# Kernel tuning notes

Hardware: AMD Instinct MI355X
Metric: run time of the kernel (lower is better)

## Reference

```python
import jax, jax.numpy as jnp
import numpy as np

NEG_SLOPE = 0.2

def setup_inputs() -> dict:
    key = jax.random.key(0)
    k1, k2, k3, k4 = jax.random.split(key, 4)
    N, K, C_IN, C_OUT = 8192, 4, 512, 512
    inputs = jax.random.normal(k1, (N, C_IN), dtype=jnp.float32)
    adj_set = jax.random.uniform(k2, (K, N, N), dtype=jnp.float32)
    att = jax.random.uniform(k3, (K,), dtype=jnp.float32)
    # xavier_uniform for w
    limit = float(np.sqrt(6.0 / (C_IN + C_OUT)))
    w = jax.random.uniform(k4, (C_IN, C_OUT), minval=-limit, maxval=limit, dtype=jnp.float32)
    b = jnp.zeros((C_OUT,), dtype=jnp.float32)
    return {"inputs": inputs, "adj_set": adj_set, "att": att, "w": w, "b": b}

def reference(inputs, adj_set, att, w, b):
    # support: [N, C_out]
    support = inputs @ w + b
    # residual=True path: outputs = sum_i att[i] * (adj_i @ support)
    #                             = (sum_i att[i] * adj_i) @ support
    combined_adj = jnp.einsum('k,knm->nm', att, adj_set)  # [N, N]
    outputs = combined_adj @ support                       # [N, C_out]
    # LeakyReLU(negative_slope=0.2)
    return jnp.where(outputs >= 0, outputs, NEG_SLOPE * outputs)
```

## Files before the change

kernel.cpp:

```cpp
#include <hip/hip_runtime.h>

#define LP  40
#define LPB 40

typedef __attribute__((ext_vector_type(8))) short short8;
typedef __attribute__((ext_vector_type(4))) short short4t;
typedef __attribute__((ext_vector_type(4))) float f32x4;

__device__ __forceinline__ short f2bf(float f) {
  unsigned u = __builtin_bit_cast(unsigned, f);
  u += 0x7FFFu + ((u >> 16) & 1u);
  return (short)(u >> 16);
}

__device__ __forceinline__ float lrelu(float v) { return v >= 0.f ? v : 0.2f * v; }

__global__ __launch_bounds__(256) void k_wt(const float* __restrict__ w,
                                            short* __restrict__ wt) {
  __shared__ float t[64][65];
  int c0 = (blockIdx.x & 7) * 64;
  int n0 = (blockIdx.x >> 3) * 64;
  int r  = threadIdx.x >> 4;
  int q4 = (threadIdx.x & 15) * 4;
  for (int i = 0; i < 4; i++) {
    int c = r + i * 16;
    f32x4 v = *(const f32x4*)(w + (size_t)(c0 + c) * 512 + (n0 + q4));
    t[c][q4 + 0] = v[0]; t[c][q4 + 1] = v[1]; t[c][q4 + 2] = v[2]; t[c][q4 + 3] = v[3];
  }
  __syncthreads();
  for (int i = 0; i < 4; i++) {
    int n = r + i * 16;
    short4t o;
    for (int j = 0; j < 4; j++) o[j] = f2bf(t[q4 + j][n]);
    *(short4t*)(wt + (size_t)(n0 + n) * 512 + (c0 + q4)) = o;
  }
}

__global__ __launch_bounds__(512, 2) void k_support(const float* __restrict__ inp,
                                                    const short* __restrict__ wt,
                                                    const float* __restrict__ bias,
                                                    short* __restrict__ sup) {
  __shared__ __align__(16) short As[512 * LP];
  __shared__ __align__(16) short Bs[64 * LP];
  const int tid = threadIdx.x;
  const int m0 = blockIdx.x * 64;
  const int wave = tid >> 6, lane = tid & 63;
  const int wn = wave >> 1, wm = wave & 1;
  const int lr = lane & 15, lk = lane >> 4;
  const int bm = tid >> 3, bk = (tid & 7) * 4;
  f32x4 acc[8][2] = {};
  short8 ar[4]; f32x4 br;
  auto loadA = [&](int s) {
    const short* p = wt + (size_t)tid * 512 + s * 32;
    ar[0] = *(const short8*)(p);      ar[1] = *(const short8*)(p + 8);
    ar[2] = *(const short8*)(p + 16); ar[3] = *(const short8*)(p + 24);
  };
  auto loadB = [&](int s) {
    br = *(const f32x4*)(inp + (size_t)(m0 + bm) * 512 + s * 32 + bk);
  };
  loadA(0); loadB(0);
  for (int s = 0; s < 16; s++) {
    short* ad = As + tid * LP;
    *(short8*)(ad) = ar[0]; *(short8*)(ad + 8) = ar[1];
    *(short8*)(ad + 16) = ar[2]; *(short8*)(ad + 24) = ar[3];
    short4t bo;
    for (int j = 0; j < 4; j++) bo[j] = f2bf(br[j]);
    *(short4t*)(Bs + bm * LP + bk) = bo;
    __syncthreads();
    if (s + 1 < 16) { loadA(s + 1); loadB(s + 1); }
    short8 af[8], bfr[2];
    for (int nf = 0; nf < 8; nf++)
      af[nf] = *(const short8*)(As + (wn * 128 + nf * 16 + lr) * LP + lk * 8);
    for (int mf = 0; mf < 2; mf++)
      bfr[mf] = *(const short8*)(Bs + (wm * 32 + mf * 16 + lr) * LP + lk * 8);
    for (int nf = 0; nf < 8; nf++)
      for (int mf = 0; mf < 2; mf++)
        acc[nf][mf] = __builtin_amdgcn_mfma_f32_16x16x32_bf16(af[nf], bfr[mf], acc[nf][mf], 0, 0, 0);
    __syncthreads();
  }
  for (int nf = 0; nf < 8; nf++) {
    int nb = wn * 128 + nf * 16 + lk * 4;
    for (int mf = 0; mf < 2; mf++) {
      int m = m0 + wm * 32 + mf * 16 + lr;
      for (int j = 0; j < 4; j++) {
        int n = nb + j;
        sup[(size_t)n * 8192 + m] = f2bf(acc[nf][mf][j] + bias[n]);
      }
    }
  }
}

#define ISSUE(SL, S) {                                                          \
    const float* p_ = abase + (size_t)(S) * 32;                                 \
    R[SL][0] = __builtin_nontemporal_load((const f32x4*)(p_));                  \
    R[SL][1] = __builtin_nontemporal_load((const f32x4*)(p_ + (1ull << 26)));   \
    R[SL][2] = __builtin_nontemporal_load((const f32x4*)(p_ + (2ull << 26)));   \
    R[SL][3] = __builtin_nontemporal_load((const f32x4*)(p_ + (3ull << 26)));   \
  }

#define ISSUEAF(SL, S) {                                                        \
    const short* q_ = supp + (size_t)(S) * 32;                                  \
    AF[SL][0] = *(const short8*)(q_);                                           \
    AF[SL][1] = *(const short8*)(q_ + (size_t)16 * 8192);                       \
    AF[SL][2] = *(const short8*)(q_ + (size_t)32 * 8192);                       \
    AF[SL][3] = *(const short8*)(q_ + (size_t)48 * 8192);                       \
  }

#define STEP(U) {                                                               \
    ISSUE(((U) + 2) & 3, (s0 + (U) + 2) & (nsteps - 1))                         \
    ISSUEAF(((U) + 1) & 1, (s0 + (U) + 1) & (nsteps - 1))                       \
    __builtin_amdgcn_sched_barrier(0);                                          \
    asm volatile("s_waitcnt vmcnt(20)" ::: "memory");                           \
    __builtin_amdgcn_sched_barrier(0);                                          \
    f32x4 c_;                                                                   \
    _Pragma("unroll") for (int e = 0; e < 4; e++)                               \
      c_[e] = t0 * R[(U) & 3][0][e] + t1 * R[(U) & 3][1][e]                     \
            + t2 * R[(U) & 3][2][e] + t3 * R[(U) & 3][3][e];                    \
    short4t o_;                                                                 \
    _Pragma("unroll") for (int e = 0; e < 4; e++) o_[e] = f2bf(c_[e]);          \
    *(short4t*)(Bs[(U) & 1] + r * LPB + q * 4) = o_;                            \
    asm volatile("s_waitcnt lgkmcnt(0)" ::: "memory");                          \
    __builtin_amdgcn_sched_barrier(0);                                          \
    __builtin_amdgcn_s_barrier();                                               \
    __builtin_amdgcn_sched_barrier(0);                                          \
    short8 bfr[4];                                                              \
    _Pragma("unroll") for (int mf = 0; mf < 4; mf++)                            \
      bfr[mf] = *(const short8*)(Bs[(U) & 1] + (mf * 16 + lr) * LPB + lk * 8);  \
    asm volatile("s_waitcnt vmcnt(8)" ::: "memory");                            \
    __builtin_amdgcn_sched_barrier(0);                                          \
    _Pragma("unroll") for (int nf = 0; nf < 4; nf++)                            \
      _Pragma("unroll") for (int mf = 0; mf < 4; mf++)                          \
        acc[nf][mf] = __builtin_amdgcn_mfma_f32_16x16x32_bf16(AF[(U) & 1][nf],  \
                          bfr[mf], acc[nf][mf], 0, 0, 0);                       \
  }

__global__ __launch_bounds__(512, 2) void k_main(const float* __restrict__ adj,
                                                 const float* __restrict__ att,
                                                 const short* __restrict__ sup,
                                                 float* __restrict__ part,
                                                 float* __restrict__ outp,
                                                 int ksplit) {
  __shared__ __align__(16) short Bs[2][64 * LPB];
  const int tid = threadIdx.x;
  const int b = blockIdx.x;
  const int xpk = 8 / ksplit;
  const int xcd = b & 7;
  const int kc = xcd / xpk;
  const int m0 = ((b >> 3) * xpk + (xcd % xpk)) * 64;
  const int kchunk = 8192 / ksplit;
  const int nsteps = kchunk / 32;
  const int kbase = kc * kchunk;
  const float t0 = att[0], t1 = att[1], t2 = att[2], t3 = att[3];
  const int wave = tid >> 6, lane = tid & 63;
  const int lr = lane & 15, lk = lane >> 4;
  const int r = tid >> 3, q = tid & 7;
  f32x4 acc[4][4] = {};
  const float* abase = adj + (size_t)(m0 + r) * 8192 + kbase + q * 4;
  const short* supp = sup + (size_t)(wave * 64 + lr) * 8192 + kbase + lk * 8;
  f32x4 R[4][4];
  short8 AF[2][4];

  ISSUE(0, 0) ISSUEAF(0, 0) ISSUE(1, 1)
  for (int s0 = 0; s0 < nsteps; s0 += 4) {
    STEP(0) STEP(1) STEP(2) STEP(3)
  }

#pragma unroll
  for (int nf = 0; nf < 4; nf++) {
    int n = wave * 64 + nf * 16 + lk * 4;
#pragma unroll
    for (int mf = 0; mf < 4; mf++) {
      int m = m0 + mf * 16 + lr;
      f32x4 v = acc[nf][mf];
      if (ksplit == 1) {
        for (int j = 0; j < 4; j++) v[j] = lrelu(v[j]);
        __builtin_nontemporal_store(v, (f32x4*)(outp + (size_t)m * 512 + n));
      } else {
        __builtin_nontemporal_store(v, (f32x4*)(part + ((size_t)kc << 22) + (size_t)m * 512 + n));
      }
    }
  }
}

__global__ __launch_bounds__(256) void k_reduce(const float* __restrict__ part,
                                                float* __restrict__ outp, int ksplit) {
  const size_t total = (size_t)8192 * 512 / 4;
  for (size_t i = (size_t)blockIdx.x * 256 + threadIdx.x; i < total;
       i += (size_t)gridDim.x * 256) {
    f32x4 a = __builtin_nontemporal_load((const f32x4*)(part + i * 4));
    for (int k = 1; k < ksplit; k++) {
      f32x4 bv = __builtin_nontemporal_load((const f32x4*)(part + ((size_t)k << 22) + i * 4));
      for (int j = 0; j < 4; j++) a[j] += bv[j];
    }
    f32x4 v;
    for (int j = 0; j < 4; j++) v[j] = lrelu(a[j]);
    __builtin_nontemporal_store(v, (f32x4*)(outp + i * 4));
  }
}

extern "C" void kernel_launch(void* const* d_in, const int* in_sizes, int n_in,
                              void* d_out, int out_size, void* d_ws, size_t ws_size,
                              hipStream_t stream) {
  const float* inputs = (const float*)d_in[0];
  const float* adj    = (const float*)d_in[1];
  const float* att    = (const float*)d_in[2];
  const float* w      = (const float*)d_in[3];
  const float* bias   = (const float*)d_in[4];
  float* outp = (float*)d_out;

  char* ws = (char*)d_ws;
  short* sup  = (short*)(ws);
  short* wt   = (short*)(ws + (8u << 20));
  float* part = (float*)(ws + (9u << 20));

  const size_t base = (9ull << 20), psz = (1ull << 24);
  int ksplit = (ws_size >= base + 2 * psz) ? 2 : 1;

  k_wt<<<64, 256, 0, stream>>>(w, wt);
  k_support<<<128, 512, 0, stream>>>(inputs, wt, bias, sup);
  k_main<<<128 * ksplit, 512, 0, stream>>>(adj, att, sup, part, outp, ksplit);
  if (ksplit > 1) k_reduce<<<1024, 256, 0, stream>>>(part, outp, ksplit);
}
```

Measured before the change: 308.1 us.

## Add 128-row tile main kernel with 4-way K split and reduction

Adds a new main kernel in which each block handles 128 output rows (instead of 64) over a quarter of the K dimension. The kernel uses a shallower two-stage register prefetch and wider 8-float adjacency loads per thread. Doubling the row tile halves how often the support matrix is re-read per adjacency byte, and the 4-way K split keeps 256 blocks in flight. The cost is more accumulator registers, a larger partial buffer, and a four-way reduction pass. The old path remains as a fallback when the workspace is too small.

```diff
diff --git a/kernel.cpp b/kernel.cpp
--- a/kernel.cpp
+++ b/kernel.cpp
@@ -90,7 +90,89 @@
   }
 }
 
-#define ISSUE(SL, S) {                                                          \
+#define ISSUEB(SL, S) {                                                         \
+    const float* p_ = abase + (size_t)(S) * 32;                                 \
+    R[SL][0][0] = __builtin_nontemporal_load((const f32x4*)(p_));               \
+    R[SL][0][1] = __builtin_nontemporal_load((const f32x4*)(p_ + 4));           \
+    R[SL][1][0] = __builtin_nontemporal_load((const f32x4*)(p_ + (1ull << 26)));\
+    R[SL][1][1] = __builtin_nontemporal_load((const f32x4*)(p_ + (1ull << 26) + 4));\
+    R[SL][2][0] = __builtin_nontemporal_load((const f32x4*)(p_ + (2ull << 26)));\
+    R[SL][2][1] = __builtin_nontemporal_load((const f32x4*)(p_ + (2ull << 26) + 4));\
+    R[SL][3][0] = __builtin_nontemporal_load((const f32x4*)(p_ + (3ull << 26)));\
+    R[SL][3][1] = __builtin_nontemporal_load((const f32x4*)(p_ + (3ull << 26) + 4));\
+  }
+
+#define STEPB(U) {                                                              \
+    const int s_ = s0 + (U);                                                    \
+    _Pragma("unroll") for (int nf = 0; nf < 4; nf++)                            \
+      AF[nf] = *(const short8*)(supp + (size_t)(nf * 16) * 8192 + (size_t)s_ * 32); \
+    ISSUEB(((U) + 1) & 1, (s_ + 1) & 63)                                        \
+    __builtin_amdgcn_sched_barrier(0);                                          \
+    asm volatile("s_waitcnt vmcnt(8)" ::: "memory");                            \
+    __builtin_amdgcn_sched_barrier(0);                                          \
+    f32x4 c0_, c1_;                                                             \
+    _Pragma("unroll") for (int e = 0; e < 4; e++) {                             \
+      c0_[e] = t0 * R[(U)][0][0][e] + t1 * R[(U)][1][0][e]                      \
+             + t2 * R[(U)][2][0][e] + t3 * R[(U)][3][0][e];                     \
+      c1_[e] = t0 * R[(U)][0][1][e] + t1 * R[(U)][1][1][e]                      \
+             + t2 * R[(U)][2][1][e] + t3 * R[(U)][3][1][e];                     \
+    }                                                                           \
+    short8 o_;                                                                  \
+    _Pragma("unroll") for (int e = 0; e < 4; e++) {                             \
+      o_[e] = f2bf(c0_[e]); o_[4 + e] = f2bf(c1_[e]);                           \
+    }                                                                           \
+    *(short8*)(Bs[(U) & 1] + r * LPB + q * 8) = o_;                             \
+    asm volatile("s_waitcnt lgkmcnt(0)" ::: "memory");                          \
+    __builtin_amdgcn_sched_barrier(0);                                          \
+    __builtin_amdgcn_s_barrier();                                               \
+    __builtin_amdgcn_sched_barrier(0);                                          \
+    _Pragma("unroll") for (int mf = 0; mf < 8; mf++) {                          \
+      short8 bfr = *(const short8*)(Bs[(U) & 1] + (mf * 16 + lr) * LPB + lk * 8); \
+      _Pragma("unroll") for (int nf = 0; nf < 4; nf++)                          \
+        acc[nf][mf] = __builtin_amdgcn_mfma_f32_16x16x32_bf16(AF[nf], bfr,      \
+                                                              acc[nf][mf], 0, 0, 0); \
+    }                                                                           \
+  }
+
+__global__ __launch_bounds__(512, 2) void k_main128(const float* __restrict__ adj,
+                                                    const float* __restrict__ att,
+                                                    const short* __restrict__ sup,
+                                                    float* __restrict__ part) {
+  __shared__ __align__(16) short Bs[2][128 * LPB];
+  const int tid = threadIdx.x;
+  const int b = blockIdx.x;
+  const int xcd = b & 7;
+  const int kc = xcd >> 1;
+  const int m0 = ((b >> 3) * 2 + (xcd & 1)) * 128;
+  const int kbase = kc * 2048;
+  const float t0 = att[0], t1 = att[1], t2 = att[2], t3 = att[3];
+  const int wave = tid >> 6, lane = tid & 63;
+  const int lr = lane & 15, lk = lane >> 4;
+  const int r = tid >> 2, q = tid & 3;
+  f32x4 acc[4][8] = {};
+  const float* abase = adj + (size_t)(m0 + r) * 8192 + kbase + q * 8;
+  const short* supp = sup + (size_t)(wave * 64 + lr) * 8192 + kbase + lk * 8;
+  f32x4 R[2][4][2];
+  short8 AF[4];
+
+  ISSUEB(0, 0)
+  for (int s0 = 0; s0 < 64; s0 += 2) {
+    STEPB(0) STEPB(1)
+  }
+
+#pragma unroll
+  for (int nf = 0; nf < 4; nf++) {
+    int n = wave * 64 + nf * 16 + lk * 4;
+#pragma unroll
+    for (int mf = 0; mf < 8; mf++) {
+      int m = m0 + mf * 16 + lr;
+      __builtin_nontemporal_store(acc[nf][mf],
+          (f32x4*)(part + ((size_t)kc << 22) + (size_t)m * 512 + n));
+    }
+  }
+}
+
+#define ISSUE64(SL, S) {                                                        \
     const float* p_ = abase + (size_t)(S) * 32;                                 \
     R[SL][0] = __builtin_nontemporal_load((const f32x4*)(p_));                  \
     R[SL][1] = __builtin_nontemporal_load((const f32x4*)(p_ + (1ull << 26)));   \
@@ -98,7 +180,7 @@
     R[SL][3] = __builtin_nontemporal_load((const f32x4*)(p_ + (3ull << 26)));   \
   }
 
-#define ISSUEAF(SL, S) {                                                        \
+#define ISSUEAF64(SL, S) {                                                      \
     const short* q_ = supp + (size_t)(S) * 32;                                  \
     AF[SL][0] = *(const short8*)(q_);                                           \
     AF[SL][1] = *(const short8*)(q_ + (size_t)16 * 8192);                       \
@@ -106,9 +188,9 @@
     AF[SL][3] = *(const short8*)(q_ + (size_t)48 * 8192);                       \
   }
 
-#define STEP(U) {                                                               \
-    ISSUE(((U) + 2) & 3, (s0 + (U) + 2) & (nsteps - 1))                         \
-    ISSUEAF(((U) + 1) & 1, (s0 + (U) + 1) & (nsteps - 1))                       \
+#define STEP64(U) {                                                             \
+    ISSUE64(((U) + 2) & 3, (s0 + (U) + 2) & (nsteps - 1))                       \
+    ISSUEAF64(((U) + 1) & 1, (s0 + (U) + 1) & (nsteps - 1))                     \
     __builtin_amdgcn_sched_barrier(0);                                          \
     asm volatile("s_waitcnt vmcnt(20)" ::: "memory");                           \
     __builtin_amdgcn_sched_barrier(0);                                          \
@@ -134,12 +216,12 @@
                           bfr[mf], acc[nf][mf], 0, 0, 0);                       \
   }
 
-__global__ __launch_bounds__(512, 2) void k_main(const float* __restrict__ adj,
-                                                 const float* __restrict__ att,
-                                                 const short* __restrict__ sup,
-                                                 float* __restrict__ part,
-                                                 float* __restrict__ outp,
-                                                 int ksplit) {
+__global__ __launch_bounds__(512, 2) void k_main64(const float* __restrict__ adj,
+                                                   const float* __restrict__ att,
+                                                   const short* __restrict__ sup,
+                                                   float* __restrict__ part,
+                                                   float* __restrict__ outp,
+                                                   int ksplit) {
   __shared__ __align__(16) short Bs[2][64 * LPB];
   const int tid = threadIdx.x;
   const int b = blockIdx.x;
@@ -160,9 +242,9 @@
   f32x4 R[4][4];
   short8 AF[2][4];
 
-  ISSUE(0, 0) ISSUEAF(0, 0) ISSUE(1, 1)
+  ISSUE64(0, 0) ISSUEAF64(0, 0) ISSUE64(1, 1)
   for (int s0 = 0; s0 < nsteps; s0 += 4) {
-    STEP(0) STEP(1) STEP(2) STEP(3)
+    STEP64(0) STEP64(1) STEP64(2) STEP64(3)
   }
 
 #pragma unroll
@@ -214,10 +296,16 @@
   float* part = (float*)(ws + (9u << 20));
 
   const size_t base = (9ull << 20), psz = (1ull << 24);
-  int ksplit = (ws_size >= base + 2 * psz) ? 2 : 1;
 
   k_wt<<<64, 256, 0, stream>>>(w, wt);
   k_support<<<128, 512, 0, stream>>>(inputs, wt, bias, sup);
-  k_main<<<128 * ksplit, 512, 0, stream>>>(adj, att, sup, part, outp, ksplit);
-  if (ksplit > 1) k_reduce<<<1024, 256, 0, stream>>>(part, outp, ksplit);
-}
+
+  if (ws_size >= base + 4 * psz) {
+    k_main128<<<256, 512, 0, stream>>>(adj, att, sup, part);
+    k_reduce<<<1024, 256, 0, stream>>>(part, outp, 4);
+  } else {
+    int ksplit = (ws_size >= base + 2 * psz) ? 2 : 1;
+    k_main64<<<128 * ksplit, 512, 0, stream>>>(adj, att, sup, part, outp, ksplit);
+    if (ksplit > 1) k_reduce<<<1024, 256, 0, stream>>>(part, outp, ksplit);
+  }
+}
```

After: 342.9 us. +11.3%, slower.

## Double K-step to 64 per iteration with wider loads and templated split

Applied to the files above, without the earlier changes.

The main GEMM loop now handles 64 columns of K per step instead of 32. Each thread loads 8 floats per adjacency slice, writes one 16-byte bf16 store into LDS, and runs twice as many MFMAs between barriers. The number of in-flight register buffers changes from 4 slots to 2, and the split factor becomes a template parameter so the step count is a compile-time constant. The intent is to halve barrier and wait overhead per unit of work and to use wider memory transactions. In exchange, register pressure rises and pipelining depth in steps drops.

```diff
diff --git a/kernel.cpp b/kernel.cpp
--- a/kernel.cpp
+++ b/kernel.cpp
@@ -1,7 +1,7 @@
 #include <hip/hip_runtime.h>
 
 #define LP  40
-#define LPB 40
+#define LPB 72
 
 typedef __attribute__((ext_vector_type(8))) short short8;
 typedef __attribute__((ext_vector_type(4))) short short4t;
@@ -90,79 +90,92 @@
   }
 }
 
-#define ISSUE(SL, S) {                                                          \
-    const float* p_ = abase + (size_t)(S) * 32;                                 \
+#define ISSUEA(SL, S) {                                                         \
+    const float* p_ = abase + (size_t)(S) * 64;                                 \
     R[SL][0] = __builtin_nontemporal_load((const f32x4*)(p_));                  \
-    R[SL][1] = __builtin_nontemporal_load((const f32x4*)(p_ + (1ull << 26)));   \
-    R[SL][2] = __builtin_nontemporal_load((const f32x4*)(p_ + (2ull << 26)));   \
-    R[SL][3] = __builtin_nontemporal_load((const f32x4*)(p_ + (3ull << 26)));   \
-  }
-
-#define ISSUEAF(SL, S) {                                                        \
-    const short* q_ = supp + (size_t)(S) * 32;                                  \
-    AF[SL][0] = *(const short8*)(q_);                                           \
-    AF[SL][1] = *(const short8*)(q_ + (size_t)16 * 8192);                       \
-    AF[SL][2] = *(const short8*)(q_ + (size_t)32 * 8192);                       \
-    AF[SL][3] = *(const short8*)(q_ + (size_t)48 * 8192);                       \
-  }
-
-#define STEP(U) {                                                               \
-    ISSUE(((U) + 2) & 3, (s0 + (U) + 2) & (nsteps - 1))                         \
-    ISSUEAF(((U) + 1) & 1, (s0 + (U) + 1) & (nsteps - 1))                       \
-    __builtin_amdgcn_sched_barrier(0);                                          \
-    asm volatile("s_waitcnt vmcnt(20)" ::: "memory");                           \
-    __builtin_amdgcn_sched_barrier(0);                                          \
-    f32x4 c_;                                                                   \
-    _Pragma("unroll") for (int e = 0; e < 4; e++)                               \
-      c_[e] = t0 * R[(U) & 3][0][e] + t1 * R[(U) & 3][1][e]                     \
-            + t2 * R[(U) & 3][2][e] + t3 * R[(U) & 3][3][e];                    \
-    short4t o_;                                                                 \
-    _Pragma("unroll") for (int e = 0; e < 4; e++) o_[e] = f2bf(c_[e]);          \
-    *(short4t*)(Bs[(U) & 1] + r * LPB + q * 4) = o_;                            \
+    R[SL][1] = __builtin_nontemporal_load((const f32x4*)(p_ + 4));              \
+    R[SL][2] = __builtin_nontemporal_load((const f32x4*)(p_ + (1ull << 26)));   \
+    R[SL][3] = __builtin_nontemporal_load((const f32x4*)(p_ + (1ull << 26) + 4));\
+    R[SL][4] = __builtin_nontemporal_load((const f32x4*)(p_ + (2ull << 26)));   \
+    R[SL][5] = __builtin_nontemporal_load((const f32x4*)(p_ + (2ull << 26) + 4));\
+    R[SL][6] = __builtin_nontemporal_load((const f32x4*)(p_ + (3ull << 26)));   \
+    R[SL][7] = __builtin_nontemporal_load((const f32x4*)(p_ + (3ull << 26) + 4));\
+  }
+
+#define ISSUEF(SL, S) {                                                         \
+    const short* q_ = supp + (size_t)(S) * 64;                                  \
+    AF[SL][0][0] = *(const short8*)(q_);                                        \
+    AF[SL][0][1] = *(const short8*)(q_ + 32);                                   \
+    AF[SL][1][0] = *(const short8*)(q_ + (size_t)16 * 8192);                    \
+    AF[SL][1][1] = *(const short8*)(q_ + (size_t)16 * 8192 + 32);               \
+    AF[SL][2][0] = *(const short8*)(q_ + (size_t)32 * 8192);                    \
+    AF[SL][2][1] = *(const short8*)(q_ + (size_t)32 * 8192 + 32);               \
+    AF[SL][3][0] = *(const short8*)(q_ + (size_t)48 * 8192);                    \
+    AF[SL][3][1] = *(const short8*)(q_ + (size_t)48 * 8192 + 32);               \
+  }
+
+#define STEPK(U) {                                                              \
+    const int s_ = s0 + (U);                                                    \
+    ISSUEF(((U) + 1) & 1, (s_ + 1) & (NSTEPS - 1))                              \
+    __builtin_amdgcn_sched_barrier(0);                                          \
+    asm volatile("s_waitcnt vmcnt(16)" ::: "memory");                           \
+    __builtin_amdgcn_sched_barrier(0);                                          \
+    f32x4 cA_, cB_;                                                             \
+    _Pragma("unroll") for (int e = 0; e < 4; e++) {                             \
+      cA_[e] = t0 * R[(U)][0][e] + t1 * R[(U)][2][e]                            \
+             + t2 * R[(U)][4][e] + t3 * R[(U)][6][e];                           \
+      cB_[e] = t0 * R[(U)][1][e] + t1 * R[(U)][3][e]                            \
+             + t2 * R[(U)][5][e] + t3 * R[(U)][7][e];                           \
+    }                                                                           \
+    short8 o_;                                                                  \
+    _Pragma("unroll") for (int e = 0; e < 4; e++) {                             \
+      o_[e] = f2bf(cA_[e]); o_[4 + e] = f2bf(cB_[e]);                           \
+    }                                                                           \
+    *(short8*)(Bs[(U)] + r * LPB + q * 8) = o_;                                 \
+    ISSUEA((U), (s_ + 2) & (NSTEPS - 1))                                        \
+    __builtin_amdgcn_sched_barrier(0);                                          \
     asm volatile("s_waitcnt lgkmcnt(0)" ::: "memory");                          \
     __builtin_amdgcn_sched_barrier(0);                                          \
     __builtin_amdgcn_s_barrier();                                               \
     __builtin_amdgcn_sched_barrier(0);                                          \
-    short8 bfr[4];                                                              \
-    _Pragma("unroll") for (int mf = 0; mf < 4; mf++)                            \
-      bfr[mf] = *(const short8*)(Bs[(U) & 1] + (mf * 16 + lr) * LPB + lk * 8);  \
-    asm volatile("s_waitcnt vmcnt(8)" ::: "memory");                            \
-    __builtin_amdgcn_sched_barrier(0);                                          \
-    _Pragma("unroll") for (int nf = 0; nf < 4; nf++)                            \
-      _Pragma("unroll") for (int mf = 0; mf < 4; mf++)                          \
-        acc[nf][mf] = __builtin_amdgcn_mfma_f32_16x16x32_bf16(AF[(U) & 1][nf],  \
-                          bfr[mf], acc[nf][mf], 0, 0, 0);                       \
-  }
-
+    _Pragma("unroll") for (int h = 0; h < 2; h++) {                             \
+      _Pragma("unroll") for (int mf = 0; mf < 4; mf++) {                        \
+        short8 bfr = *(const short8*)(Bs[(U)] + (mf * 16 + lr) * LPB + h * 32 + lk * 8); \
+        _Pragma("unroll") for (int nf = 0; nf < 4; nf++)                        \
+          acc[nf][mf] = __builtin_amdgcn_mfma_f32_16x16x32_bf16(                \
+              AF[(U)][nf][h], bfr, acc[nf][mf], 0, 0, 0);                       \
+      }                                                                         \
+    }                                                                           \
+  }
+
+template <int KSPLIT>
 __global__ __launch_bounds__(512, 2) void k_main(const float* __restrict__ adj,
                                                  const float* __restrict__ att,
                                                  const short* __restrict__ sup,
                                                  float* __restrict__ part,
-                                                 float* __restrict__ outp,
-                                                 int ksplit) {
+                                                 float* __restrict__ outp) {
+  constexpr int NSTEPS = 8192 / KSPLIT / 64;
   __shared__ __align__(16) short Bs[2][64 * LPB];
   const int tid = threadIdx.x;
   const int b = blockIdx.x;
-  const int xpk = 8 / ksplit;
+  const int xpk = 8 / KSPLIT;
   const int xcd = b & 7;
   const int kc = xcd / xpk;
   const int m0 = ((b >> 3) * xpk + (xcd % xpk)) * 64;
-  const int kchunk = 8192 / ksplit;
-  const int nsteps = kchunk / 32;
-  const int kbase = kc * kchunk;
+  const int kbase = kc * (8192 / KSPLIT);
   const float t0 = att[0], t1 = att[1], t2 = att[2], t3 = att[3];
   const int wave = tid >> 6, lane = tid & 63;
   const int lr = lane & 15, lk = lane >> 4;
   const int r = tid >> 3, q = tid & 7;
   f32x4 acc[4][4] = {};
-  const float* abase = adj + (size_t)(m0 + r) * 8192 + kbase + q * 4;
+  const float* abase = adj + (size_t)(m0 + r) * 8192 + kbase + q * 8;
   const short* supp = sup + (size_t)(wave * 64 + lr) * 8192 + kbase + lk * 8;
-  f32x4 R[4][4];
-  short8 AF[2][4];
-
-  ISSUE(0, 0) ISSUEAF(0, 0) ISSUE(1, 1)
-  for (int s0 = 0; s0 < nsteps; s0 += 4) {
-    STEP(0) STEP(1) STEP(2) STEP(3)
+  f32x4 R[2][8];
+  short8 AF[2][4][2];
+
+  ISSUEA(0, 0) ISSUEF(0, 0) ISSUEA(1, 1)
+  for (int s0 = 0; s0 < NSTEPS; s0 += 2) {
+    STEPK(0) STEPK(1)
   }
 
 #pragma unroll
@@ -172,7 +185,7 @@
     for (int mf = 0; mf < 4; mf++) {
       int m = m0 + mf * 16 + lr;
       f32x4 v = acc[nf][mf];
-      if (ksplit == 1) {
+      if (KSPLIT == 1) {
         for (int j = 0; j < 4; j++) v[j] = lrelu(v[j]);
         __builtin_nontemporal_store(v, (f32x4*)(outp + (size_t)m * 512 + n));
       } else {
@@ -214,10 +227,14 @@
   float* part = (float*)(ws + (9u << 20));
 
   const size_t base = (9ull << 20), psz = (1ull << 24);
-  int ksplit = (ws_size >= base + 2 * psz) ? 2 : 1;
 
   k_wt<<<64, 256, 0, stream>>>(w, wt);
   k_support<<<128, 512, 0, stream>>>(inputs, wt, bias, sup);
-  k_main<<<128 * ksplit, 512, 0, stream>>>(adj, att, sup, part, outp, ksplit);
-  if (ksplit > 1) k_reduce<<<1024, 256, 0, stream>>>(part, outp, ksplit);
-}
+
+  if (ws_size >= base + 2 * psz) {
+    k_main<2><<<256, 512, 0, stream>>>(adj, att, sup, part, outp);
+    k_reduce<<<1024, 256, 0, stream>>>(part, outp, 2);
+  } else {
+    k_main<1><<<128, 512, 0, stream>>>(adj, att, sup, part, outp);
+  }
+}
```

After: 336.9 us. 1.09x slower.

## Add producer/consumer warp-specialized main kernel using global-to-LDS loads

Applied to the files above, without the earlier changes.

Adds a new main kernel in which wave 0 streams the four adjacency slices straight into a 4-slot LDS ring with global_load_lds, while the other waves wait on shared flags, combine the slices with the attention weights, convert to bf16 and run MFMAs. Counters in LDS tell the producer when a slot is free. The aim is to hide HBM latency for the 1 GiB adjacency stream without staging it through registers, and to spread the combine work across all waves. The risks are spin-wait overhead, a single producer wave possibly limiting load issue rate, and 128 KB of LDS per block, which may cut occupancy below the two blocks the launch bounds request.

```diff
diff --git a/kernel.cpp b/kernel.cpp
--- a/kernel.cpp
+++ b/kernel.cpp
@@ -90,25 +90,144 @@
   }
 }
 
-#define ISSUE(SL, S) {                                                          \
+__global__ __launch_bounds__(512, 2) void k_pc(const float* __restrict__ adj,
+                                               const float* __restrict__ att,
+                                               const short* __restrict__ sup,
+                                               float* __restrict__ part) {
+  constexpr int NSTEPS = 128;
+  __shared__ __align__(16) float ring[4][8192];
+  __shared__ int flg[4];
+  __shared__ int done[4];
+  const int tid = threadIdx.x;
+  const int b = blockIdx.x;
+  const int xcd = b & 7;
+  const int kc = xcd >> 2;
+  const int m0 = ((b >> 3) * 4 + (xcd & 3)) * 64;
+  const int kbase = kc * 4096;
+  const float t0 = att[0], t1 = att[1], t2 = att[2], t3 = att[3];
+  const int wv = tid >> 6, lane = tid & 63;
+  const int lr = lane & 15, lk = lane >> 4;
+  const int swz = (lane & 7) << 4;
+  volatile int* vflg = flg;
+  volatile int* vdone = done;
+
+  if (tid < 4) { flg[tid] = 0; done[tid] = 0; }
+  __syncthreads();
+
+  const short* sb = sup + (size_t)(wv * 64 + lr) * 8192 + kbase + lk * 8;
+  f32x4 acc[4][4] = {};
+  short8 af[4], afn[4];
+
+  const int lr8 = lane >> 3, l7 = lane & 7;
+  const float* pbase = adj + (size_t)(m0 + lr8) * 8192 + kbase + (l7 ^ lr8) * 4;
+
+#define PISSUE(S, SLOT)                                                        \
+  _Pragma("unroll") for (int c = 0; c < 32; c++) {                             \
+    const float* g_ = pbase + (((size_t)(c >> 3)) << 26)                       \
+                    + (size_t)((c & 7) * 8) * 8192 + (size_t)(S) * 32;         \
+    __builtin_amdgcn_global_load_lds(                                          \
+        (const __attribute__((address_space(1))) unsigned*)g_,                 \
+        (__attribute__((address_space(3))) unsigned*)((char*)ring[SLOT] + c * 1024), \
+        16, 0, 0);                                                             \
+  }
+
+#define LOADAF(DST, S)                                                         \
+  _Pragma("unroll") for (int nf = 0; nf < 4; nf++)                             \
+    DST[nf] = *(const short8*)(sb + (size_t)(nf * 16) * 8192 + (size_t)(S) * 32);
+
+#define CONSUME(S, AFC)                                                        \
+  {                                                                            \
+    const char* rb_ = (const char*)ring[(S) & 3];                              \
+    _Pragma("unroll") for (int mf = 0; mf < 4; mf++) {                         \
+      const char* rr_ = rb_ + (mf * 16 + lr) * 128;                            \
+      const int o0_ = (lk * 32) ^ swz, o1_ = (lk * 32 + 16) ^ swz;             \
+      f32x4 r0a = *(const f32x4*)(rr_ + o0_);                                  \
+      f32x4 r0b = *(const f32x4*)(rr_ + o1_);                                  \
+      f32x4 r1a = *(const f32x4*)(rr_ + 8192 + o0_);                           \
+      f32x4 r1b = *(const f32x4*)(rr_ + 8192 + o1_);                           \
+      f32x4 r2a = *(const f32x4*)(rr_ + 16384 + o0_);                          \
+      f32x4 r2b = *(const f32x4*)(rr_ + 16384 + o1_);                          \
+      f32x4 r3a = *(const f32x4*)(rr_ + 24576 + o0_);                          \
+      f32x4 r3b = *(const f32x4*)(rr_ + 24576 + o1_);                          \
+      short8 bfr_;                                                             \
+      _Pragma("unroll") for (int e = 0; e < 4; e++) {                          \
+        bfr_[e]     = f2bf(t0 * r0a[e] + t1 * r1a[e] + t2 * r2a[e] + t3 * r3a[e]); \
+        bfr_[4 + e] = f2bf(t0 * r0b[e] + t1 * r1b[e] + t2 * r2b[e] + t3 * r3b[e]); \
+      }                                                                        \
+      _Pragma("unroll") for (int nf = 0; nf < 4; nf++)                         \
+        acc[nf][mf] = __builtin_amdgcn_mfma_f32_16x16x32_bf16(AFC[nf], bfr_,   \
+                                                              acc[nf][mf], 0, 0, 0); \
+    }                                                                          \
+  }
+
+  if (wv == 0) {
+    PISSUE(0, 0)
+    LOADAF(af, 0)
+    for (int s = 0; s < NSTEPS; s++) {
+      const int sn = s + 1;
+      if (sn < NSTEPS) {
+        const int slot = sn & 3;
+        const int need = 7 * (sn >> 2);
+        while (vdone[slot] < need) __builtin_amdgcn_s_sleep(2);
+        asm volatile("" ::: "memory");
+        PISSUE(sn, slot)
+        LOADAF(afn, sn)
+        asm volatile("s_waitcnt vmcnt(36)" ::: "memory");
+      } else {
+        asm volatile("s_waitcnt vmcnt(0)" ::: "memory");
+      }
+      vflg[s & 3] = s + 1;
+      asm volatile("" ::: "memory");
+      CONSUME(s, af)
+#pragma unroll
+      for (int nf = 0; nf < 4; nf++) af[nf] = afn[nf];
+    }
+  } else {
+    LOADAF(af, 0)
+    for (int s = 0; s < NSTEPS; s++) {
+      if (s + 1 < NSTEPS) LOADAF(afn, s + 1)
+      while (vflg[s & 3] != s + 1) __builtin_amdgcn_s_sleep(2);
+      asm volatile("" ::: "memory");
+      CONSUME(s, af)
+      asm volatile("" ::: "memory");
+      if (lane == 0) atomicAdd(&done[s & 3], 1);
+#pragma unroll
+      for (int nf = 0; nf < 4; nf++) af[nf] = afn[nf];
+    }
+  }
+
+#pragma unroll
+  for (int nf = 0; nf < 4; nf++) {
+    int n = wv * 64 + nf * 16 + lk * 4;
+#pragma unroll
+    for (int mf = 0; mf < 4; mf++) {
+      int m = m0 + mf * 16 + lr;
+      __builtin_nontemporal_store(acc[nf][mf],
+          (f32x4*)(part + ((size_t)kc << 22) + (size_t)m * 512 + n));
+    }
+  }
+#undef PISSUE
+#undef LOADAF
+#undef CONSUME
+}
+
+#define ISSUE64(SL, S) {                                                        \
     const float* p_ = abase + (size_t)(S) * 32;                                 \
     R[SL][0] = __builtin_nontemporal_load((const f32x4*)(p_));                  \
     R[SL][1] = __builtin_nontemporal_load((const f32x4*)(p_ + (1ull << 26)));   \
     R[SL][2] = __builtin_nontemporal_load((const f32x4*)(p_ + (2ull << 26)));   \
     R[SL][3] = __builtin_nontemporal_load((const f32x4*)(p_ + (3ull << 26)));   \
   }
-
-#define ISSUEAF(SL, S) {                                                        \
+#define ISSUEAF64(SL, S) {                                                      \
     const short* q_ = supp + (size_t)(S) * 32;                                  \
     AF[SL][0] = *(const short8*)(q_);                                           \
     AF[SL][1] = *(const short8*)(q_ + (size_t)16 * 8192);                       \
     AF[SL][2] = *(const short8*)(q_ + (size_t)32 * 8192);                       \
     AF[SL][3] = *(const short8*)(q_ + (size_t)48 * 8192);                       \
   }
-
-#define STEP(U) {                                                               \
-    ISSUE(((U) + 2) & 3, (s0 + (U) + 2) & (nsteps - 1))                         \
-    ISSUEAF(((U) + 1) & 1, (s0 + (U) + 1) & (nsteps - 1))                       \
+#define STEP64(U) {                                                             \
+    ISSUE64(((U) + 2) & 3, (s0 + (U) + 2) & (nsteps - 1))                       \
+    ISSUEAF64(((U) + 1) & 1, (s0 + (U) + 1) & (nsteps - 1))                     \
     __builtin_amdgcn_sched_barrier(0);                                          \
     asm volatile("s_waitcnt vmcnt(20)" ::: "memory");                           \
     __builtin_amdgcn_sched_barrier(0);                                          \
@@ -134,12 +253,12 @@
                           bfr[mf], acc[nf][mf], 0, 0, 0);                       \
   }
 
-__global__ __launch_bounds__(512, 2) void k_main(const float* __restrict__ adj,
-                                                 const float* __restrict__ att,
-                                                 const short* __restrict__ sup,
-                                                 float* __restrict__ part,
-                                                 float* __restrict__ outp,
-                                                 int ksplit) {
+__global__ __launch_bounds__(512, 2) void k_main64(const float* __restrict__ adj,
+                                                   const float* __restrict__ att,
+                                                   const short* __restrict__ sup,
+                                                   float* __restrict__ part,
+                                                   float* __restrict__ outp,
+                                                   int ksplit) {
   __shared__ __align__(16) short Bs[2][64 * LPB];
   const int tid = threadIdx.x;
   const int b = blockIdx.x;
@@ -159,12 +278,10 @@
   const short* supp = sup + (size_t)(wave * 64 + lr) * 8192 + kbase + lk * 8;
   f32x4 R[4][4];
   short8 AF[2][4];
-
-  ISSUE(0, 0) ISSUEAF(0, 0) ISSUE(1, 1)
+  ISSUE64(0, 0) ISSUEAF64(0, 0) ISSUE64(1, 1)
   for (int s0 = 0; s0 < nsteps; s0 += 4) {
-    STEP(0) STEP(1) STEP(2) STEP(3)
-  }
-
+    STEP64(0) STEP64(1) STEP64(2) STEP64(3)
+  }
 #pragma unroll
   for (int nf = 0; nf < 4; nf++) {
     int n = wave * 64 + nf * 16 + lk * 4;
@@ -214,10 +331,14 @@
   float* part = (float*)(ws + (9u << 20));
 
   const size_t base = (9ull << 20), psz = (1ull << 24);
-  int ksplit = (ws_size >= base + 2 * psz) ? 2 : 1;
 
   k_wt<<<64, 256, 0, stream>>>(w, wt);
   k_support<<<128, 512, 0, stream>>>(inputs, wt, bias, sup);
-  k_main<<<128 * ksplit, 512, 0, stream>>>(adj, att, sup, part, outp, ksplit);
-  if (ksplit > 1) k_reduce<<<1024, 256, 0, stream>>>(part, outp, ksplit);
-}
+
+  if (ws_size >= base + 2 * psz) {
+    k_pc<<<256, 512, 0, stream>>>(adj, att, sup, part);
+    k_reduce<<<1024, 256, 0, stream>>>(part, outp, 2);
+  } else {
+    k_main64<<<128, 512, 0, stream>>>(adj, att, sup, part, outp, 1);
+  }
+}
```

New measurement: 350.1 us. 13.7% more time.
